# Optimization experiments

Hardware: AMD Instinct MI355X
Metric: run time of the kernel (lower is better)

## Reference

```python
import jax, jax.numpy as jnp
import numpy as np
from jax import lax

N = 30000   # total nodes in batched graph
E = 240000  # total edges
D = 64      # embed_dim
IN = 128    # in_dim
G = 64      # number of graphs
L = 2       # num_layers (EdgePooling layers)
C = 10      # num_class
NEG = jnp.float32(-1e30)


def _edge_pool_layer(x, edge_index, node_mask, edge_mask, W, b):
    """One PyG EdgePooling layer on fixed-size (masked) node/edge arrays.

    x: [N, D] node features (inactive slots are zero)
    edge_index: [2, E] int32 (invalid edges masked by edge_mask)
    Returns new (x, edge_index, node_mask, edge_mask) with same static shapes.
    """
    src, dst = edge_index[0], edge_index[1]
    # raw edge score: Linear(2D -> 1) on cat(x[src], x[dst])
    feat = jnp.concatenate([x[src], x[dst]], axis=-1)               # [E, 2D]
    raw = feat @ W + b                                              # [E]
    # softmax grouped by target node (PyG compute_edge_score_softmax)
    r = jnp.where(edge_mask, raw, NEG)
    m = jax.ops.segment_max(r, dst, num_segments=N)                 # [N]
    ex = jnp.where(edge_mask, jnp.exp(r - m[dst]), 0.0)
    den = jax.ops.segment_sum(ex, dst, num_segments=N)
    score = ex / jnp.maximum(den[dst], 1e-16)
    e_plus = score + 0.5                                            # add_to_edge_score

    # greedy edge contraction in descending score order (sequential by nature)
    order = jnp.argsort(jnp.where(edge_mask, -e_plus, jnp.inf)).astype(jnp.int32)
    so, to, mo = src[order], dst[order], edge_mask[order]

    def step(carry, inp):
        avail, cluster, picked = carry
        s, t, em, eid = inp
        ok = em & avail[s] & avail[t]   # s==t (self-loop) handled: same slot
        avail = avail.at[s].set(avail[s] & ~ok)
        avail = avail.at[t].set(avail[t] & ~ok)
        cluster = cluster.at[t].set(jnp.where(ok, s, cluster[t]))
        picked = picked.at[s].set(jnp.where(ok, eid, picked[s]))
        return (avail, cluster, picked), None

    init = (node_mask,
            jnp.arange(N, dtype=jnp.int32),       # cluster rep = source slot
            jnp.full((N,), E, dtype=jnp.int32))   # sentinel E = 'not merged'
    (avail, cluster, picked), _ = lax.scan(step, init, (so, to, mo, order))

    # merged clusters get their edge score, singletons get 1.0
    e_pad = jnp.concatenate([e_plus, jnp.ones((1,), e_plus.dtype)])
    mult = e_pad[picked]                                            # [N]
    new_x = jax.ops.segment_sum(x, cluster, num_segments=N) * mult[:, None]
    new_node_mask = jax.ops.segment_max(node_mask.astype(jnp.int32), cluster,
                                        num_segments=N) > 0

    # remap + coalesce edges (dedup, keep self-loops as PyG does)
    ns, nt = cluster[src], cluster[dst]
    key = jnp.where(edge_mask, ns * N + nt, N * N)  # fits int32 for N=30000
    perm = jnp.argsort(key)
    sk = key[perm]
    first = jnp.concatenate([jnp.array([True]), sk[1:] != sk[:-1]])
    keep = first & (sk < N * N)
    new_edge_mask = jnp.zeros((E,), bool).at[perm].set(keep)
    new_edge_index = jnp.stack([ns, nt])
    return new_x, new_edge_index, new_node_mask, new_edge_mask


def setup_inputs() -> dict:
    key = jax.random.key(0)
    ks = jax.random.split(key, 6)
    x = jax.random.normal(ks[0], (N, IN), jnp.float32)
    edge_index = jax.random.randint(ks[1], (2, E), 0, N, dtype=jnp.int32)
    batch = jnp.sort(jax.random.randint(ks[2], (N,), 0, G, dtype=jnp.int32))
    W_embed = jax.random.normal(ks[3], (IN, D), jnp.float32) / np.sqrt(IN)
    We = jax.random.normal(ks[4], (L, 2 * D), jnp.float32) / np.sqrt(2 * D)
    be = jnp.zeros((L,), jnp.float32)
    W_fc = jax.random.normal(ks[5], (D * (L + 1), C), jnp.float32) / np.sqrt(D * (L + 1))
    b_fc = jnp.zeros((C,), jnp.float32)
    return {"x": x, "edge_index": edge_index, "batch": batch,
            "W_embed": W_embed, "We": We, "be": be,
            "W_fc": W_fc, "b_fc": b_fc}


def reference(x, edge_index, batch, W_embed, We, be, W_fc, b_fc):
    z = x @ W_embed                                   # node_embed (Linear, no bias)
    node_mask = jnp.ones((N,), bool)
    edge_mask = jnp.ones((E,), bool)
    embs = [jax.ops.segment_sum(z, batch, num_segments=G)]   # global_add_pool
    ei = edge_index
    for l in range(L):
        z, ei, node_mask, edge_mask = _edge_pool_layer(z, ei, node_mask, edge_mask,
                                                       We[l], be[l])
        embs.append(jax.ops.segment_sum(z, batch, num_segments=G))
    Z = jnp.concatenate(embs, axis=1)                 # [G, D*(L+1)]
    return Z @ W_fc + b_fc                            # [G, C]
```

## Files before the change

### kernel.cpp

```cpp
#include <hip/hip_runtime.h>
#include <math.h>

#define kN 30000
#define kE 240000
#define kG 64
#define kHSZ (1 << 19)
#define kMB 64
#define kMT 1024
#define kGSZ (kMB * kMT)
#define kCAP 4
#define kSMALL 8192

typedef unsigned long long ull;
#define kDEAD (~0ULL)

__device__ __forceinline__ int ald(const int* p) {
  return __hip_atomic_load(p, __ATOMIC_RELAXED, __HIP_MEMORY_SCOPE_AGENT);
}
__device__ __forceinline__ ull aldull(const ull* p) {
  return __hip_atomic_load(p, __ATOMIC_RELAXED, __HIP_MEMORY_SCOPE_AGENT);
}
__device__ __forceinline__ void astull(ull* p, ull v) {
  __hip_atomic_store(p, v, __ATOMIC_RELAXED, __HIP_MEMORY_SCOPE_AGENT);
}
__device__ __forceinline__ void amax64(ull* p, ull v) {
  __hip_atomic_fetch_max(p, v, __ATOMIC_RELAXED, __HIP_MEMORY_SCOPE_AGENT);
}
__device__ __forceinline__ ull wldull(const ull* p) {
  return __hip_atomic_load(p, __ATOMIC_RELAXED, __HIP_MEMORY_SCOPE_WORKGROUP);
}
__device__ __forceinline__ void wstull(ull* p, ull v) {
  __hip_atomic_store(p, v, __ATOMIC_RELAXED, __HIP_MEMORY_SCOPE_WORKGROUP);
}
__device__ __forceinline__ void wmax64(ull* p, ull v) {
  __hip_atomic_fetch_max(p, v, __ATOMIC_RELAXED, __HIP_MEMORY_SCOPE_WORKGROUP);
}
__device__ __forceinline__ unsigned enc_f(float x) {
  unsigned u = __float_as_uint(x);
  return (u & 0x80000000u) ? ~u : (u | 0x80000000u);
}
__device__ __forceinline__ float dec_f(unsigned u) {
  u = (u & 0x80000000u) ? (u ^ 0x80000000u) : ~u;
  return __uint_as_float(u);
}
__device__ __forceinline__ ull mk_key(int r, unsigned enc, int e) {
  return ((ull)r << 50) | ((ull)enc << 18) | (ull)(262143 - e);
}

__device__ __forceinline__ void round_bar(int* bar, int* gen) {
  __syncthreads();
  if (threadIdx.x == 0) {
    int g = ++(*gen);
    __hip_atomic_fetch_add(bar, 1, __ATOMIC_ACQ_REL, __HIP_MEMORY_SCOPE_AGENT);
    while (__hip_atomic_load(bar, __ATOMIC_ACQUIRE, __HIP_MEMORY_SCOPE_AGENT) < kMB * g)
      __builtin_amdgcn_s_sleep(2);
  }
  __syncthreads();
}

__global__ __launch_bounds__(256) void k_embed(const float* __restrict__ x,
                                               const float* __restrict__ W,
                                               float* __restrict__ z) {
  __shared__ float sW[128 * 64];
  int tid = threadIdx.x;
  for (int i = tid; i < 128 * 64; i += 256) sW[i] = W[i];
  __syncthreads();
  int lane = tid & 63, sub = tid >> 6;
  int row0 = blockIdx.x * 16;
  for (int r = sub; r < 16; r += 4) {
    int n = row0 + r;
    if (n >= kN) continue;
    const float* xr = x + (size_t)n * 128;
    float acc = 0.f;
#pragma unroll
    for (int k = 0; k < 128; ++k) acc = fmaf(xr[k], sW[k * 64 + lane], acc);
    z[(size_t)n * 64 + lane] = acc;
  }
}

__global__ void k_init(int* __restrict__ cluster, int* __restrict__ partner,
                       float* __restrict__ mult, double* __restrict__ den,
                       ull* __restrict__ best, int* __restrict__ cnt,
                       int* __restrict__ ctrl, int* __restrict__ hkey,
                       int* __restrict__ hmin, float* __restrict__ embs,
                       int layer1) {
  int S = gridDim.x * blockDim.x;
  for (int i = blockIdx.x * blockDim.x + threadIdx.x; i < kHSZ; i += S) {
    if (i < kN) {
      cluster[i] = i;
      partner[i] = -1;
      mult[i] = 1.f;
      den[i] = 0.0;
    }
    if (i < 2 * kN) best[i] = 0ULL;
    if (i < 16384) cnt[i] = 0;
    if (i < 8) ctrl[i] = 0;
    if (layer1) {
      hkey[i] = -1;
      hmin[i] = 0x7fffffff;
      if (i < 3 * kG * 64) embs[i] = 0.f;
    }
  }
}

__global__ __launch_bounds__(1024) void k_ab(const float* __restrict__ z,
                                             const float* __restrict__ We,
                                             int layer, float* __restrict__ a,
                                             float* __restrict__ b) {
  int wid = (blockIdx.x * 1024 + threadIdx.x) >> 6;
  int lane = threadIdx.x & 63;
  int nw = (gridDim.x * 1024) >> 6;
  float wlo = We[layer * 128 + lane];
  float whi = We[layer * 128 + 64 + lane];
  for (int n = wid; n < kN; n += nw) {
    float zv = z[(size_t)n * 64 + lane];
    float fa = zv * wlo, fb = zv * whi;
#pragma unroll
    for (int m = 32; m > 0; m >>= 1) {
      fa += __shfl_xor(fa, m, 64);
      fb += __shfl_xor(fb, m, 64);
    }
    if (lane == 0) {
      a[n] = fa;
      b[n] = fb;
    }
  }
}

__global__ void k_rawe(const float* __restrict__ a, const float* __restrict__ b,
                       const float* __restrict__ be, int layer,
                       const int* __restrict__ esrc, const int* __restrict__ edst,
                       const int* __restrict__ emask, float* __restrict__ raws,
                       double* __restrict__ den) {
  int e = blockIdx.x * 256 + threadIdx.x;
  if (e >= kE) return;
  if (emask && !emask[e]) return;
  int t = edst[e];
  float raw = a[esrc[e]] + b[t] + be[layer];
  raws[e] = raw;
  atomicAdd(&den[t], exp((double)raw));
}

__global__ __launch_bounds__(kMT) void k_match_mw(
    const int* __restrict__ esrc, const int* __restrict__ edst,
    const float* __restrict__ raws, const int* __restrict__ emask,
    const double* __restrict__ den, ull* __restrict__ best,
    int4* __restrict__ wl, int4* __restrict__ wlB, int* __restrict__ ctrl,
    int* __restrict__ cnt, int* __restrict__ cluster, int* __restrict__ partner,
    float* __restrict__ mult) {
  const int tid = threadIdx.x;
  const int gtid = blockIdx.x * kMT + tid;
  const int lane = tid & 63;
  int gen = 0;

  int es[kCAP], et[kCAP], ee[kCAP];
  unsigned en[kCAP];
  int myc = 0;
#pragma unroll
  for (int k = 0; k < kCAP; ++k) {
    ee[k] = -1;
    int e = gtid + k * kGSZ;
    if (e >= kE) continue;
    if (emask && !emask[e]) continue;
    int s = esrc[e], t = edst[e];
    double ex = exp((double)raws[e]);
    float ep = (float)(ex / den[t]) + 0.5f;
    unsigned u = enc_f(ep);
    es[k] = s; et[k] = t; en[k] = u; ee[k] = e;
    ++myc;
    ull key = mk_key(1, u, e);
    if (key > best[kN + s]) amax64(&best[kN + s], key);
    if (t != s && key > best[kN + t]) amax64(&best[kN + t], key);
  }
  {
    int a = myc;
#pragma unroll
    for (int m = 32; m; m >>= 1) a += __shfl_xor(a, m, 64);
    if (lane == 0 && a)
      __hip_atomic_fetch_add(&cnt[0], a, __ATOMIC_RELAXED, __HIP_MEMORY_SCOPE_AGENT);
  }

  int r = 1;
  bool to_tail = false;
  for (; r < 8000; ++r) {
    round_bar(&ctrl[0], &gen);
    int tot = ald(&cnt[r - 1]);
    if (tot == 0) return;
    if (tot < kSMALL) { to_tail = true; break; }
    ull* bchk = best + (size_t)(r & 1) * kN;
    ull* bpost = best + (size_t)((r + 1) & 1) * kN;
    int alive = 0;
#pragma unroll
    for (int k = 0; k < kCAP; ++k) {
      if (ee[k] < 0) continue;
      int s = es[k], t = et[k];
      ull bs = aldull(&bchk[s]);
      ull bt = (t == s) ? bs : aldull(&bchk[t]);
      if (bs == kDEAD || bt == kDEAD) { ee[k] = -1; continue; }
      ull key = mk_key(r, en[k], ee[k]);
      if (bs == key && bt == key) {
        astull(&bchk[s], kDEAD);
        astull(&bpost[s], kDEAD);
        if (t != s) { astull(&bchk[t], kDEAD); astull(&bpost[t], kDEAD); }
        cluster[t] = s;
        partner[s] = t;
        mult[s] = dec_f(en[k]);
        ee[k] = -1;
      } else {
        ull k2 = mk_key(r + 1, en[k], ee[k]);
        amax64(&bpost[s], k2);
        if (t != s) amax64(&bpost[t], k2);
        ++alive;
      }
    }
    int a = alive;
#pragma unroll
    for (int m = 32; m; m >>= 1) a += __shfl_xor(a, m, 64);
    if (lane == 0 && a)
      __hip_atomic_fetch_add(&cnt[r], a, __ATOMIC_RELAXED, __HIP_MEMORY_SCOPE_AGENT);
  }
  if (!to_tail) return;

#pragma unroll
  for (int k = 0; k < kCAP; ++k) {
    bool act = (ee[k] >= 0);
    unsigned long long mb = __ballot(act);
    if (!mb) continue;
    int leader = __ffsll(mb) - 1;
    int base = 0;
    if (lane == leader)
      base = __hip_atomic_fetch_add(&ctrl[1], (int)__popcll(mb), __ATOMIC_RELAXED,
                                    __HIP_MEMORY_SCOPE_AGENT);
    base = __shfl(base, leader, 64);
    if (act)
      wl[base + __popcll(mb & ((1ULL << lane) - 1))] =
          make_int4(es[k], et[k], (int)en[k], ee[k]);
  }
  round_bar(&ctrl[0], &gen);
  if (blockIdx.x != 0) return;

  __shared__ int ls;
  int n = ald(&ctrl[1]);
  int4* cur = wl;
  int4* nxt = wlB;
  for (int rr = r; n > 0 && rr < 16300; ++rr) {
    if (tid == 0) ls = 0;
    __syncthreads();
    ull* bchk = best + (size_t)(rr & 1) * kN;
    ull* bpost = best + (size_t)((rr + 1) & 1) * kN;
    for (int i = tid; i < n; i += kMT) {
      int4 E = cur[i];
      int ss = E.x, tt = E.y, e = E.w;
      unsigned u = (unsigned)E.z;
      ull bs = wldull(&bchk[ss]);
      ull bt = (tt == ss) ? bs : wldull(&bchk[tt]);
      if (bs == kDEAD || bt == kDEAD) continue;
      ull key = mk_key(rr, u, e);
      if (bs == key && bt == key) {
        wstull(&bchk[ss], kDEAD);
        wstull(&bpost[ss], kDEAD);
        if (tt != ss) { wstull(&bchk[tt], kDEAD); wstull(&bpost[tt], kDEAD); }
        cluster[tt] = ss;
        partner[ss] = tt;
        mult[ss] = dec_f(u);
      } else {
        ull k2 = mk_key(rr + 1, u, e);
        wmax64(&bpost[ss], k2);
        if (tt != ss) wmax64(&bpost[tt], k2);
        int p = atomicAdd(&ls, 1);
        nxt[p] = E;
      }
    }
    __syncthreads();
    n = ls;
    int4* tmp = cur;
    cur = nxt;
    nxt = tmp;
  }
}

__global__ __launch_bounds__(256) void k_newx_pool(
    const float* __restrict__ z, const int* __restrict__ cluster,
    const int* __restrict__ partner, const float* __restrict__ mult,
    const int* __restrict__ batch, float* __restrict__ zo,
    float* __restrict__ embs_g) {
  int tid = threadIdx.x;
  int d = tid & 63;
  int n0 = blockIdx.x * 128 + (tid >> 6) * 32;
  float acc = 0.f;
  int curg = -1;
  for (int k = 0; k < 32; ++k) {
    int n = n0 + k;
    if (n >= kN) break;
    int g = batch[n];
    if (g != curg) {
      if (curg >= 0 && acc != 0.f) atomicAdd(&embs_g[curg * 64 + d], acc);
      acc = 0.f;
      curg = g;
    }
    float v;
    if (cluster) {
      v = 0.f;
      if (cluster[n] == n) {
        v = z[(size_t)n * 64 + d];
        int p = partner[n];
        if (p >= 0 && p != n) v += z[(size_t)p * 64 + d];
        v *= mult[n];
      }
    } else {
      v = z[(size_t)n * 64 + d];
    }
    if (zo) zo[(size_t)n * 64 + d] = v;
    acc += v;
  }
  if (curg >= 0 && acc != 0.f) atomicAdd(&embs_g[curg * 64 + d], acc);
}

__global__ void k_remap(const int* __restrict__ esrc, const int* __restrict__ edst,
                        const int* __restrict__ cluster, const int* __restrict__ emask,
                        int* __restrict__ esrcn, int* __restrict__ edstn,
                        int* __restrict__ hkey, int* __restrict__ hmin,
                        int* __restrict__ hslot) {
  int e = blockIdx.x * 256 + threadIdx.x;
  if (e >= kE) return;
  int ns = cluster[esrc[e]];
  int nt = cluster[edst[e]];
  esrcn[e] = ns;
  edstn[e] = nt;
  if (emask && !emask[e]) return;
  int key = ns * kN + nt;
  unsigned h = (((unsigned)key * 2654435761u) >> 13) & (kHSZ - 1);
  while (true) {
    int old = atomicCAS(&hkey[h], -1, key);
    if (old == -1 || old == key) break;
    h = (h + 1) & (kHSZ - 1);
  }
  atomicMin(&hmin[h], e);
  hslot[e] = (int)h;
}

__global__ void k_dedup(const int* __restrict__ emask, const int* __restrict__ hmin,
                        const int* __restrict__ hslot, int* __restrict__ emaskn) {
  int e = blockIdx.x * 256 + threadIdx.x;
  if (e >= kE) return;
  int keep = 0;
  if (!emask || emask[e]) keep = (hmin[hslot[e]] == e) ? 1 : 0;
  emaskn[e] = keep;
}

__global__ void k_final(const float* __restrict__ embs, const float* __restrict__ Wfc,
                        const float* __restrict__ bfc, float* __restrict__ out) {
  int tid = threadIdx.x;
  if (tid >= kG * 10) return;
  int g = tid / 10, c = tid % 10;
  float acc = bfc[c];
  for (int l = 0; l < 3; ++l)
    for (int d = 0; d < 64; ++d)
      acc += embs[l * (kG * 64) + g * 64 + d] * Wfc[(l * 64 + d) * 10 + c];
  out[g * 10 + c] = acc;
}

extern "C" void kernel_launch(void* const* d_in, const int* in_sizes, int n_in,
                              void* d_out, int out_size, void* d_ws, size_t ws_size,
                              hipStream_t stream) {
  (void)in_sizes; (void)n_in; (void)out_size; (void)ws_size;
  const float* x = (const float*)d_in[0];
  const int* ei = (const int*)d_in[1];
  const int* batch = (const int*)d_in[2];
  const float* Wemb = (const float*)d_in[3];
  const float* We = (const float*)d_in[4];
  const float* be = (const float*)d_in[5];
  const float* Wfc = (const float*)d_in[6];
  const float* bfc = (const float*)d_in[7];
  float* out = (float*)d_out;

  char* ws = (char*)d_ws;
  size_t off = 0;
  auto alloc = [&](size_t bytes) -> void* {
    void* p = ws + off;
    off = (off + bytes + 255) & ~(size_t)255;
    return p;
  };
  float* z0 = (float*)alloc((size_t)kN * 64 * 4);
  float* z1 = (float*)alloc((size_t)kN * 64 * 4);
  float* raws = (float*)alloc((size_t)kE * 4);
  float* an = (float*)alloc((size_t)kN * 4);
  float* bn = (float*)alloc((size_t)kN * 4);
  double* den = (double*)alloc((size_t)kN * 8);
  ull* best = (ull*)alloc((size_t)2 * kN * 8);
  int* cluster = (int*)alloc((size_t)kN * 4);
  int* partner = (int*)alloc((size_t)kN * 4);
  float* mult = (float*)alloc((size_t)kN * 4);
  int* esrc1 = (int*)alloc((size_t)kE * 4);
  int* edst1 = (int*)alloc((size_t)kE * 4);
  int* emask1 = (int*)alloc((size_t)kE * 4);
  int4* wl = (int4*)alloc((size_t)kSMALL * 16);
  int4* wlB = (int4*)alloc((size_t)kSMALL * 16);
  int* hkey = (int*)alloc((size_t)kHSZ * 4);
  int* hmin = (int*)alloc((size_t)kHSZ * 4);
  int* hslot = (int*)alloc((size_t)kE * 4);
  float* embs = (float*)alloc((size_t)3 * kG * 64 * 4);
  int* cnt = (int*)alloc((size_t)16384 * 4);
  int* ctrl = (int*)alloc(256);

  const int gE = (kE + 255) / 256;
  const int gNP = (kN + 127) / 128;

  k_init<<<512, 256, 0, stream>>>(cluster, partner, mult, den, best, cnt, ctrl,
                                  hkey, hmin, embs, 1);
  k_embed<<<kN / 16, 256, 0, stream>>>(x, Wemb, z0);
  k_newx_pool<<<gNP, 256, 0, stream>>>(z0, nullptr, nullptr, nullptr, batch, nullptr,
                                       embs);
  k_ab<<<480, 1024, 0, stream>>>(z0, We, 0, an, bn);
  k_rawe<<<gE, 256, 0, stream>>>(an, bn, be, 0, ei, ei + kE, nullptr, raws, den);
  k_match_mw<<<kMB, kMT, 0, stream>>>(ei, ei + kE, raws, nullptr, den, best, wl, wlB,
                                      ctrl, cnt, cluster, partner, mult);
  k_newx_pool<<<gNP, 256, 0, stream>>>(z0, cluster, partner, mult, batch, z1,
                                       embs + kG * 64);
  k_remap<<<gE, 256, 0, stream>>>(ei, ei + kE, cluster, nullptr, esrc1, edst1, hkey,
                                  hmin, hslot);
  k_dedup<<<gE, 256, 0, stream>>>(nullptr, hmin, hslot, emask1);

  k_init<<<512, 256, 0, stream>>>(cluster, partner, mult, den, best, cnt, ctrl,
                                  hkey, hmin, embs, 0);
  k_ab<<<480, 1024, 0, stream>>>(z1, We, 1, an, bn);
  k_rawe<<<gE, 256, 0, stream>>>(an, bn, be, 1, esrc1, edst1, emask1, raws, den);
  k_match_mw<<<kMB, kMT, 0, stream>>>(esrc1, edst1, raws, emask1, den, best, wl, wlB,
                                      ctrl, cnt, cluster, partner, mult);
  k_newx_pool<<<gNP, 256, 0, stream>>>(z1, cluster, partner, mult, batch, nullptr,
                                       embs + 2 * kG * 64);

  k_final<<<1, 640, 0, stream>>>(embs, Wfc, bfc, out);
}
```

Baseline: 1.085 ms.

## Replace multi-block greedy matching with single-workgroup LDS matching over compacted worklist

Drops the 64-block persistent matching kernel that used global 64-bit atomic keys and a software grid barrier every round. A separate kernel now computes edge scores and compacts live edges into a worklist. A single 1024-thread workgroup then runs local-max matching with 32-bit score keys and a node-availability bitmap, both held in LDS, and settles ties by minimum edge id. This removes cross-block barrier and global atomic costs, but all 240k edges are handled by one workgroup, which limits parallelism. The per-thread candidate masks (4×64 bits) assume at most 256 worklist items per thread.

```diff
diff --git a/kernel.cpp b/kernel.cpp
--- a/kernel.cpp
+++ b/kernel.cpp
@@ -5,36 +5,12 @@
 #define kE 240000
 #define kG 64
 #define kHSZ (1 << 19)
-#define kMB 64
+#define kNW 938
 #define kMT 1024
-#define kGSZ (kMB * kMT)
-#define kCAP 4
-#define kSMALL 8192
+#define kSlices 235
 
 typedef unsigned long long ull;
-#define kDEAD (~0ULL)
-
-__device__ __forceinline__ int ald(const int* p) {
-  return __hip_atomic_load(p, __ATOMIC_RELAXED, __HIP_MEMORY_SCOPE_AGENT);
-}
-__device__ __forceinline__ ull aldull(const ull* p) {
-  return __hip_atomic_load(p, __ATOMIC_RELAXED, __HIP_MEMORY_SCOPE_AGENT);
-}
-__device__ __forceinline__ void astull(ull* p, ull v) {
-  __hip_atomic_store(p, v, __ATOMIC_RELAXED, __HIP_MEMORY_SCOPE_AGENT);
-}
-__device__ __forceinline__ void amax64(ull* p, ull v) {
-  __hip_atomic_fetch_max(p, v, __ATOMIC_RELAXED, __HIP_MEMORY_SCOPE_AGENT);
-}
-__device__ __forceinline__ ull wldull(const ull* p) {
-  return __hip_atomic_load(p, __ATOMIC_RELAXED, __HIP_MEMORY_SCOPE_WORKGROUP);
-}
-__device__ __forceinline__ void wstull(ull* p, ull v) {
-  __hip_atomic_store(p, v, __ATOMIC_RELAXED, __HIP_MEMORY_SCOPE_WORKGROUP);
-}
-__device__ __forceinline__ void wmax64(ull* p, ull v) {
-  __hip_atomic_fetch_max(p, v, __ATOMIC_RELAXED, __HIP_MEMORY_SCOPE_WORKGROUP);
-}
+
 __device__ __forceinline__ unsigned enc_f(float x) {
   unsigned u = __float_as_uint(x);
   return (u & 0x80000000u) ? ~u : (u | 0x80000000u);
@@ -42,20 +18,6 @@
 __device__ __forceinline__ float dec_f(unsigned u) {
   u = (u & 0x80000000u) ? (u ^ 0x80000000u) : ~u;
   return __uint_as_float(u);
-}
-__device__ __forceinline__ ull mk_key(int r, unsigned enc, int e) {
-  return ((ull)r << 50) | ((ull)enc << 18) | (ull)(262143 - e);
-}
-
-__device__ __forceinline__ void round_bar(int* bar, int* gen) {
-  __syncthreads();
-  if (threadIdx.x == 0) {
-    int g = ++(*gen);
-    __hip_atomic_fetch_add(bar, 1, __ATOMIC_ACQ_REL, __HIP_MEMORY_SCOPE_AGENT);
-    while (__hip_atomic_load(bar, __ATOMIC_ACQUIRE, __HIP_MEMORY_SCOPE_AGENT) < kMB * g)
-      __builtin_amdgcn_s_sleep(2);
-  }
-  __syncthreads();
 }
 
 __global__ __launch_bounds__(256) void k_embed(const float* __restrict__ x,
@@ -80,8 +42,7 @@
 
 __global__ void k_init(int* __restrict__ cluster, int* __restrict__ partner,
                        float* __restrict__ mult, double* __restrict__ den,
-                       ull* __restrict__ best, int* __restrict__ cnt,
-                       int* __restrict__ ctrl, int* __restrict__ hkey,
+                       int* __restrict__ cnt, int* __restrict__ hkey,
                        int* __restrict__ hmin, float* __restrict__ embs,
                        int layer1) {
   int S = gridDim.x * blockDim.x;
@@ -92,9 +53,7 @@
       mult[i] = 1.f;
       den[i] = 0.0;
     }
-    if (i < 2 * kN) best[i] = 0ULL;
-    if (i < 16384) cnt[i] = 0;
-    if (i < 8) ctrl[i] = 0;
+    if (i < 8) cnt[i] = 0;
     if (layer1) {
       hkey[i] = -1;
       hmin[i] = 0x7fffffff;
@@ -141,141 +100,144 @@
   atomicAdd(&den[t], exp((double)raw));
 }
 
-__global__ __launch_bounds__(kMT) void k_match_mw(
-    const int* __restrict__ esrc, const int* __restrict__ edst,
-    const float* __restrict__ raws, const int* __restrict__ emask,
-    const double* __restrict__ den, ull* __restrict__ best,
-    int4* __restrict__ wl, int4* __restrict__ wlB, int* __restrict__ ctrl,
-    int* __restrict__ cnt, int* __restrict__ cluster, int* __restrict__ partner,
-    float* __restrict__ mult) {
-  const int tid = threadIdx.x;
-  const int gtid = blockIdx.x * kMT + tid;
-  const int lane = tid & 63;
-  int gen = 0;
-
-  int es[kCAP], et[kCAP], ee[kCAP];
-  unsigned en[kCAP];
-  int myc = 0;
-#pragma unroll
-  for (int k = 0; k < kCAP; ++k) {
-    ee[k] = -1;
-    int e = gtid + k * kGSZ;
-    if (e >= kE) continue;
-    if (emask && !emask[e]) continue;
+__global__ void k_score(const float* __restrict__ raws, const double* __restrict__ den,
+                        const int* __restrict__ esrc, const int* __restrict__ edst,
+                        const int* __restrict__ emask, int4* __restrict__ wl,
+                        int* __restrict__ cnt) {
+  int e = blockIdx.x * 256 + threadIdx.x;
+  int lane = threadIdx.x & 63;
+  bool live = false;
+  int st = 0;
+  unsigned u = 0;
+  if (e < kE && (!emask || emask[e])) {
     int s = esrc[e], t = edst[e];
     double ex = exp((double)raws[e]);
     float ep = (float)(ex / den[t]) + 0.5f;
-    unsigned u = enc_f(ep);
-    es[k] = s; et[k] = t; en[k] = u; ee[k] = e;
-    ++myc;
-    ull key = mk_key(1, u, e);
-    if (key > best[kN + s]) amax64(&best[kN + s], key);
-    if (t != s && key > best[kN + t]) amax64(&best[kN + t], key);
-  }
-  {
-    int a = myc;
-#pragma unroll
-    for (int m = 32; m; m >>= 1) a += __shfl_xor(a, m, 64);
-    if (lane == 0 && a)
-      __hip_atomic_fetch_add(&cnt[0], a, __ATOMIC_RELAXED, __HIP_MEMORY_SCOPE_AGENT);
-  }
-
-  int r = 1;
-  bool to_tail = false;
-  for (; r < 8000; ++r) {
-    round_bar(&ctrl[0], &gen);
-    int tot = ald(&cnt[r - 1]);
-    if (tot == 0) return;
-    if (tot < kSMALL) { to_tail = true; break; }
-    ull* bchk = best + (size_t)(r & 1) * kN;
-    ull* bpost = best + (size_t)((r + 1) & 1) * kN;
-    int alive = 0;
-#pragma unroll
-    for (int k = 0; k < kCAP; ++k) {
-      if (ee[k] < 0) continue;
-      int s = es[k], t = et[k];
-      ull bs = aldull(&bchk[s]);
-      ull bt = (t == s) ? bs : aldull(&bchk[t]);
-      if (bs == kDEAD || bt == kDEAD) { ee[k] = -1; continue; }
-      ull key = mk_key(r, en[k], ee[k]);
-      if (bs == key && bt == key) {
-        astull(&bchk[s], kDEAD);
-        astull(&bpost[s], kDEAD);
-        if (t != s) { astull(&bchk[t], kDEAD); astull(&bpost[t], kDEAD); }
-        cluster[t] = s;
-        partner[s] = t;
-        mult[s] = dec_f(en[k]);
-        ee[k] = -1;
-      } else {
-        ull k2 = mk_key(r + 1, en[k], ee[k]);
-        amax64(&bpost[s], k2);
-        if (t != s) amax64(&bpost[t], k2);
-        ++alive;
-      }
-    }
-    int a = alive;
-#pragma unroll
-    for (int m = 32; m; m >>= 1) a += __shfl_xor(a, m, 64);
-    if (lane == 0 && a)
-      __hip_atomic_fetch_add(&cnt[r], a, __ATOMIC_RELAXED, __HIP_MEMORY_SCOPE_AGENT);
-  }
-  if (!to_tail) return;
-
-#pragma unroll
-  for (int k = 0; k < kCAP; ++k) {
-    bool act = (ee[k] >= 0);
-    unsigned long long mb = __ballot(act);
-    if (!mb) continue;
+    u = enc_f(ep);
+    st = s | (t << 16);
+    live = true;
+  }
+  ull mb = __ballot(live);
+  if (mb) {
     int leader = __ffsll(mb) - 1;
     int base = 0;
-    if (lane == leader)
-      base = __hip_atomic_fetch_add(&ctrl[1], (int)__popcll(mb), __ATOMIC_RELAXED,
-                                    __HIP_MEMORY_SCOPE_AGENT);
+    if (lane == leader) base = atomicAdd(cnt, __popcll(mb));
     base = __shfl(base, leader, 64);
-    if (act)
-      wl[base + __popcll(mb & ((1ULL << lane) - 1))] =
-          make_int4(es[k], et[k], (int)en[k], ee[k]);
-  }
-  round_bar(&ctrl[0], &gen);
-  if (blockIdx.x != 0) return;
-
-  __shared__ int ls;
-  int n = ald(&ctrl[1]);
-  int4* cur = wl;
+    if (live)
+      wl[base + __popcll(mb & ((1ULL << lane) - 1))] = make_int4(st, e, (int)u, 0);
+  }
+}
+
+__global__ __launch_bounds__(kMT) void k_matchL(int4* __restrict__ wlA,
+                                                int4* __restrict__ wlB,
+                                                const int* __restrict__ cnt,
+                                                int* __restrict__ cluster,
+                                                int* __restrict__ partner,
+                                                float* __restrict__ mult) {
+  extern __shared__ unsigned dsm[];
+  unsigned* best = dsm;
+  unsigned* avail = dsm + kN;
+  __shared__ int sh_n, sh_out;
+  const int tid = threadIdx.x;
+  const int lane = tid & 63;
+
+  for (int i = tid; i < kN; i += kMT) best[i] = 0u;
+  for (int w = tid; w < kNW; w += kMT) {
+    int rem = kN - (w << 5);
+    avail[w] = (rem >= 32) ? 0xFFFFFFFFu : ((1u << rem) - 1u);
+  }
+  if (tid == 0) sh_n = cnt[0];
+  __syncthreads();
+  int n = sh_n;
+  int4* cur = wlA;
   int4* nxt = wlB;
-  for (int rr = r; n > 0 && rr < 16300; ++rr) {
-    if (tid == 0) ls = 0;
-    __syncthreads();
-    ull* bchk = best + (size_t)(rr & 1) * kN;
-    ull* bpost = best + (size_t)((rr + 1) & 1) * kN;
-    for (int i = tid; i < n; i += kMT) {
-      int4 E = cur[i];
-      int ss = E.x, tt = E.y, e = E.w;
-      unsigned u = (unsigned)E.z;
-      ull bs = wldull(&bchk[ss]);
-      ull bt = (tt == ss) ? bs : wldull(&bchk[tt]);
-      if (bs == kDEAD || bt == kDEAD) continue;
-      ull key = mk_key(rr, u, e);
-      if (bs == key && bt == key) {
-        wstull(&bchk[ss], kDEAD);
-        wstull(&bpost[ss], kDEAD);
-        if (tt != ss) { wstull(&bchk[tt], kDEAD); wstull(&bpost[tt], kDEAD); }
-        cluster[tt] = ss;
-        partner[ss] = tt;
-        mult[ss] = dec_f(u);
-      } else {
-        ull k2 = mk_key(rr + 1, u, e);
-        wmax64(&bpost[ss], k2);
-        if (tt != ss) wmax64(&bpost[tt], k2);
-        int p = atomicAdd(&ls, 1);
-        nxt[p] = E;
-      }
-    }
-    __syncthreads();
-    n = ls;
+
+  for (int round = 0; round < 4000 && n > 0; ++round) {
+    const int K = (n + kMT - 1) / kMT;
+    for (int k = 0; k < K; ++k) {
+      int i = tid + k * kMT;
+      if (i < n) {
+        int4 q = cur[i];
+        int s = q.x & 0xFFFF, t = q.x >> 16;
+        if (((avail[s >> 5] >> (s & 31)) & 1u) &&
+            ((avail[t >> 5] >> (t & 31)) & 1u)) {
+          unsigned u = (unsigned)q.z;
+          atomicMax(&best[s], u);
+          if (t != s) atomicMax(&best[t], u);
+        }
+      }
+    }
+    __syncthreads();
+    ull liveM[4] = {0, 0, 0, 0}, candM[4] = {0, 0, 0, 0}, matM[4] = {0, 0, 0, 0};
+    for (int k = 0; k < K; ++k) {
+      int i = tid + k * kMT;
+      if (i < n) {
+        int4 q = cur[i];
+        int s = q.x & 0xFFFF, t = q.x >> 16;
+        if (((avail[s >> 5] >> (s & 31)) & 1u) &&
+            ((avail[t >> 5] >> (t & 31)) & 1u)) {
+          liveM[k >> 6] |= 1ULL << (k & 63);
+          unsigned u = (unsigned)q.z;
+          if (best[s] == u && best[t] == u) candM[k >> 6] |= 1ULL << (k & 63);
+        }
+      }
+    }
+    __syncthreads();
+    for (int k = 0; k < K; ++k) {
+      if ((candM[k >> 6] >> (k & 63)) & 1ULL) {
+        int4 q = cur[tid + k * kMT];
+        int s = q.x & 0xFFFF, t = q.x >> 16;
+        atomicMin(&best[s], (unsigned)q.y);
+        if (t != s) atomicMin(&best[t], (unsigned)q.y);
+      }
+    }
+    __syncthreads();
+    for (int k = 0; k < K; ++k) {
+      if ((candM[k >> 6] >> (k & 63)) & 1ULL) {
+        int4 q = cur[tid + k * kMT];
+        int s = q.x & 0xFFFF, t = q.x >> 16;
+        if (best[s] == (unsigned)q.y && best[t] == (unsigned)q.y) {
+          matM[k >> 6] |= 1ULL << (k & 63);
+          atomicAnd(&avail[s >> 5], ~(1u << (s & 31)));
+          atomicAnd(&avail[t >> 5], ~(1u << (t & 31)));
+          cluster[t] = s;
+          partner[s] = t;
+          mult[s] = dec_f((unsigned)q.z);
+        }
+      }
+    }
+    if (tid == 0) sh_out = 0;
+    __syncthreads();
+    for (int k = 0; k < K; ++k) {
+      int i = tid + k * kMT;
+      bool surv = false;
+      int4 q = make_int4(0, 0, 0, 0);
+      if (i < n) {
+        q = cur[i];
+        int s = q.x & 0xFFFF, t = q.x >> 16;
+        best[s] = 0u;
+        best[t] = 0u;
+        bool lv = ((liveM[k >> 6] >> (k & 63)) & 1ULL) &&
+                  !((matM[k >> 6] >> (k & 63)) & 1ULL);
+        if (lv && ((avail[s >> 5] >> (s & 31)) & 1u) &&
+            ((avail[t >> 5] >> (t & 31)) & 1u))
+          surv = true;
+      }
+      ull mb = __ballot(surv);
+      if (mb) {
+        int leader = __ffsll(mb) - 1;
+        int base = 0;
+        if (lane == leader) base = atomicAdd(&sh_out, __popcll(mb));
+        base = __shfl(base, leader, 64);
+        if (surv) nxt[base + __popcll(mb & ((1ULL << lane) - 1))] = q;
+      }
+    }
+    __syncthreads();
+    n = sh_out;
     int4* tmp = cur;
     cur = nxt;
     nxt = tmp;
+    __syncthreads();
   }
 }
 
@@ -387,46 +349,45 @@
   float* an = (float*)alloc((size_t)kN * 4);
   float* bn = (float*)alloc((size_t)kN * 4);
   double* den = (double*)alloc((size_t)kN * 8);
-  ull* best = (ull*)alloc((size_t)2 * kN * 8);
   int* cluster = (int*)alloc((size_t)kN * 4);
   int* partner = (int*)alloc((size_t)kN * 4);
   float* mult = (float*)alloc((size_t)kN * 4);
   int* esrc1 = (int*)alloc((size_t)kE * 4);
   int* edst1 = (int*)alloc((size_t)kE * 4);
   int* emask1 = (int*)alloc((size_t)kE * 4);
-  int4* wl = (int4*)alloc((size_t)kSMALL * 16);
-  int4* wlB = (int4*)alloc((size_t)kSMALL * 16);
+  int4* wl0 = (int4*)alloc((size_t)kE * 16);
+  int4* wl1 = (int4*)alloc((size_t)kE * 16);
   int* hkey = (int*)alloc((size_t)kHSZ * 4);
   int* hmin = (int*)alloc((size_t)kHSZ * 4);
   int* hslot = (int*)alloc((size_t)kE * 4);
   float* embs = (float*)alloc((size_t)3 * kG * 64 * 4);
-  int* cnt = (int*)alloc((size_t)16384 * 4);
-  int* ctrl = (int*)alloc(256);
+  int* cnt = (int*)alloc(256);
 
   const int gE = (kE + 255) / 256;
   const int gNP = (kN + 127) / 128;
-
-  k_init<<<512, 256, 0, stream>>>(cluster, partner, mult, den, best, cnt, ctrl,
-                                  hkey, hmin, embs, 1);
+  const unsigned ldsBytes = (kN + kNW) * 4;
+
+  k_init<<<512, 256, 0, stream>>>(cluster, partner, mult, den, cnt, hkey, hmin,
+                                  embs, 1);
   k_embed<<<kN / 16, 256, 0, stream>>>(x, Wemb, z0);
   k_newx_pool<<<gNP, 256, 0, stream>>>(z0, nullptr, nullptr, nullptr, batch, nullptr,
                                        embs);
   k_ab<<<480, 1024, 0, stream>>>(z0, We, 0, an, bn);
   k_rawe<<<gE, 256, 0, stream>>>(an, bn, be, 0, ei, ei + kE, nullptr, raws, den);
-  k_match_mw<<<kMB, kMT, 0, stream>>>(ei, ei + kE, raws, nullptr, den, best, wl, wlB,
-                                      ctrl, cnt, cluster, partner, mult);
+  k_score<<<gE, 256, 0, stream>>>(raws, den, ei, ei + kE, nullptr, wl0, cnt);
+  k_matchL<<<1, kMT, ldsBytes, stream>>>(wl0, wl1, cnt, cluster, partner, mult);
   k_newx_pool<<<gNP, 256, 0, stream>>>(z0, cluster, partner, mult, batch, z1,
                                        embs + kG * 64);
   k_remap<<<gE, 256, 0, stream>>>(ei, ei + kE, cluster, nullptr, esrc1, edst1, hkey,
                                   hmin, hslot);
   k_dedup<<<gE, 256, 0, stream>>>(nullptr, hmin, hslot, emask1);
 
-  k_init<<<512, 256, 0, stream>>>(cluster, partner, mult, den, best, cnt, ctrl,
-                                  hkey, hmin, embs, 0);
+  k_init<<<512, 256, 0, stream>>>(cluster, partner, mult, den, cnt, hkey, hmin,
+                                  embs, 0);
   k_ab<<<480, 1024, 0, stream>>>(z1, We, 1, an, bn);
   k_rawe<<<gE, 256, 0, stream>>>(an, bn, be, 1, esrc1, edst1, emask1, raws, den);
-  k_match_mw<<<kMB, kMT, 0, stream>>>(esrc1, edst1, raws, emask1, den, best, wl, wlB,
-                                      ctrl, cnt, cluster, partner, mult);
+  k_score<<<gE, 256, 0, stream>>>(raws, den, esrc1, edst1, emask1, wl0, cnt);
+  k_matchL<<<1, kMT, ldsBytes, stream>>>(wl0, wl1, cnt, cluster, partner, mult);
   k_newx_pool<<<gNP, 256, 0, stream>>>(z1, cluster, partner, mult, batch, nullptr,
                                        embs + 2 * kG * 64);
 
```

Measured after the change: 2.903 ms. 168% more time.
